# Kernel optimization log

Measured on AMD Instinct MI355X. Metric: run time of the kernel, lower is better.

## Reference

```python
import jax, jax.numpy as jnp
import numpy as np
import math

B, S, H, NH = 8, 1024, 1024, 16
DK = H // NH
EPS = 1e-6


def setup_inputs() -> dict:
    key = jax.random.key(0)
    ks = jax.random.split(key, 8)
    enc = jax.random.normal(ks[0], (B, S, H), dtype=jnp.float32)
    mask = jax.random.randint(ks[1], (B, 1, S, S), 0, 2, dtype=jnp.int32)
    scale = 1.0 / math.sqrt(H)
    W_Q = jax.random.normal(ks[2], (H, H), dtype=jnp.float32) * scale
    W_K = jax.random.normal(ks[3], (H, H), dtype=jnp.float32) * scale
    W_V = jax.random.normal(ks[4], (H, H), dtype=jnp.float32) * scale
    W_O = jax.random.normal(ks[5], (H, H), dtype=jnp.float32) * scale
    ln_gamma = jnp.ones((H,), dtype=jnp.float32)
    ln_beta = jnp.zeros((H,), dtype=jnp.float32)
    return {"enc": enc, "mask": mask, "W_Q": W_Q, "W_K": W_K, "W_V": W_V,
            "W_O": W_O, "ln_gamma": ln_gamma, "ln_beta": ln_beta}


def _layer_norm(x, gamma, beta):
    mu = jnp.mean(x, axis=-1, keepdims=True)
    var = jnp.mean(jnp.square(x - mu), axis=-1, keepdims=True)
    return (x - mu) / jnp.sqrt(var + EPS) * gamma + beta


def reference(enc, mask, W_Q, W_K, W_V, W_O, ln_gamma, ln_beta):
    # torch Linear: y = x @ W.T  (bias=False)
    # [B,S,H] -> [B,NH,S,DK]
    def heads(x, W):
        y = jnp.einsum('bsh,oh->bso', x, W)
        return y.reshape(B, S, NH, DK).transpose(0, 2, 1, 3)
    Q = heads(enc, W_Q)
    K = heads(enc, W_K)
    V = heads(enc, W_V)
    # attention scores [B,NH,S,S]
    scores = jnp.einsum('bhqd,bhkd->bhqk', Q, K) / math.sqrt(DK)
    scores = jnp.where(mask == 0, jnp.float32(-1e9), scores)
    attn_dist = jax.nn.softmax(scores, axis=-1)  # dropout_rate=0 -> no-op
    out = jnp.einsum('bhqk,bhkd->bhqd', attn_dist, V)
    out = out.transpose(0, 2, 1, 3).reshape(B, S, H)
    out = jnp.einsum('bsh,oh->bso', out, W_O)
    out = _layer_norm(out + enc, ln_gamma, ln_beta)
    return (out, attn_dist)
```

## Files before the change

kernel.cpp:

```cpp
#include <hip/hip_runtime.h>
#include <hip/hip_bf16.h>


typedef __bf16 bf16;
typedef __attribute__((ext_vector_type(8))) __bf16 bf16x8;
typedef __attribute__((ext_vector_type(4))) __bf16 bf16x4;
typedef __attribute__((ext_vector_type(4))) float f32x4;

#define MFMA16(a, b, c) __builtin_amdgcn_mfma_f32_16x16x32_bf16((a), (b), (c), 0, 0, 0)

#define B_ 8
#define S_ 1024
#define NH_ 16
#define DK_ 64
#define H_ 1024

#define SBAR()                                             \
  {                                                        \
    asm volatile("s_waitcnt lgkmcnt(0)" ::: "memory");     \
    __builtin_amdgcn_sched_barrier(0);                     \
    __builtin_amdgcn_s_barrier();                          \
    __builtin_amdgcn_sched_barrier(0);                     \
  }

__device__ __forceinline__ void gload_lds16b(const void* g, void* l) {
  __builtin_amdgcn_global_load_lds(
      (__attribute__((address_space(1))) void*)g,
      (__attribute__((address_space(3))) void*)l, 16, 0, 0);
}

__device__ __forceinline__ bf16x8 cat8(bf16x4 a, bf16x4 b) {
  bf16x8 r;
  r[0] = a[0]; r[1] = a[1]; r[2] = a[2]; r[3] = a[3];
  r[4] = b[0]; r[5] = b[1]; r[6] = b[2]; r[7] = b[3];
  return r;
}

__global__ __launch_bounds__(256) void cvt_all_kern(const float* __restrict__ enc,
                                                    const float* __restrict__ wq,
                                                    const float* __restrict__ wk,
                                                    const float* __restrict__ wv,
                                                    const float* __restrict__ wo_in,
                                                    const int* __restrict__ mask,
                                                    bf16* __restrict__ enc_bf,
                                                    bf16* __restrict__ wqkv,
                                                    bf16* __restrict__ wo,
                                                    unsigned char* __restrict__ mask8) {
  int i = blockIdx.x * 256 + threadIdx.x;
  if (i < 2097152) {
    float4 v = ((const float4*)enc)[i];
    bf16x4 o;
    o[0] = (bf16)v.x; o[1] = (bf16)v.y; o[2] = (bf16)v.z; o[3] = (bf16)v.w;
    ((bf16x4*)enc_bf)[i] = o;
  } else if (i < 3145728) {
    int j = i - 2097152;
    const float* src;
    bf16* dst;
    if (j < 262144) { src = wq; dst = (bf16*)wqkv; }
    else if (j < 524288) { src = wk; dst = wqkv + 1048576; j -= 262144; }
    else if (j < 786432) { src = wv; dst = wqkv + 2097152; j -= 524288; }
    else { src = wo_in; dst = wo; j -= 786432; }
    float4 v = ((const float4*)src)[j];
    bf16x4 o;
    o[0] = (bf16)v.x; o[1] = (bf16)v.y; o[2] = (bf16)v.z; o[3] = (bf16)v.w;
    ((bf16x4*)dst)[j] = o;
  } else {
    int j = i - 3145728;
    int4 v = ((const int4*)mask)[j];
    uchar4 o;
    o.x = (unsigned char)v.x; o.y = (unsigned char)v.y;
    o.z = (unsigned char)v.z; o.w = (unsigned char)v.w;
    ((uchar4*)mask8)[j] = o;
  }
}

__global__ __launch_bounds__(512, 2) void gemm256_kern(const bf16* __restrict__ A,
                                                       const bf16* __restrict__ Bt,
                                                       bf16* __restrict__ C,
                                                       int N, int NT) {
  __shared__ char Ab[2][32768];
  __shared__ char Bb[2][32768];
  const int nwg = gridDim.x;
  const int chunk = nwg >> 3;
  const int lin = blockIdx.x;
  const int v = (lin & 7) * chunk + (lin >> 3);
  const int tm = v / NT, tn = v % NT;
  const size_t m0 = (size_t)tm * 256, n0 = (size_t)tn * 256;
  const int t = threadIdx.x;
  const int l = t & 63, l15 = l & 15, lg = l >> 4;
  const int w = t >> 6, wr = w >> 2, wc = w & 3;

  const int row_t = t >> 3;
  const int scol = (((t & 7) ^ (row_t & 7)) << 4);
  const size_t Kb = 2048;
  const char* Ag = (const char*)A + (m0 + row_t) * Kb + scol;
  const char* Bg = (const char*)Bt + (n0 + row_t) * Kb + scol;
  const int dst = t * 16;

#define STAGE256(kt, buf)                                                        \
  {                                                                              \
    const size_t ko = (size_t)(kt) * 128;                                        \
    _Pragma("unroll") for (int ld = 0; ld < 4; ld++)                             \
        gload_lds16b(Ag + (size_t)ld * 64 * Kb + ko, &Ab[buf][ld * 8192 + dst]); \
    _Pragma("unroll") for (int ld = 0; ld < 4; ld++)                             \
        gload_lds16b(Bg + (size_t)ld * 64 * Kb + ko, &Bb[buf][ld * 8192 + dst]); \
  }

  const int sw = (l15 & 7) << 4;
  const int arowb = wr * 16384 + l15 * 128;
  const int browb = wc * 8192 + l15 * 128;

  f32x4 acc[8][4] = {};

  STAGE256(0, 0);
  STAGE256(1, 1);
  asm volatile("s_waitcnt vmcnt(8)" ::: "memory");
  __builtin_amdgcn_sched_barrier(0);
  __builtin_amdgcn_s_barrier();

  for (int it = 0; it < 16; ++it) {
    const int buf = it & 1;
#pragma unroll
    for (int kk = 0; kk < 2; kk++) {
      bf16x8 a[8], b[4];
#pragma unroll
      for (int i = 0; i < 8; i++)
        a[i] = *(const bf16x8*)&Ab[buf][arowb + i * 2048 + ((kk * 64 + lg * 16) ^ sw)];
#pragma unroll
      for (int n = 0; n < 4; n++)
        b[n] = *(const bf16x8*)&Bb[buf][browb + n * 2048 + ((kk * 64 + lg * 16) ^ sw)];
      __builtin_amdgcn_s_setprio(1);
#pragma unroll
      for (int i = 0; i < 8; i++)
#pragma unroll
        for (int n = 0; n < 4; n++) acc[i][n] = MFMA16(a[i], b[n], acc[i][n]);
      __builtin_amdgcn_s_setprio(0);
    }
    asm volatile("s_waitcnt lgkmcnt(0)" ::: "memory");
    __builtin_amdgcn_sched_barrier(0);
    __builtin_amdgcn_s_barrier();
    if (it < 14) STAGE256(it + 2, buf);
    if (it < 15) {
      if (it == 14) {
        asm volatile("s_waitcnt vmcnt(0)" ::: "memory");
      } else {
        asm volatile("s_waitcnt vmcnt(8)" ::: "memory");
      }
      __builtin_amdgcn_sched_barrier(0);
      __builtin_amdgcn_s_barrier();
    }
  }

#pragma unroll
  for (int i = 0; i < 8; i++)
#pragma unroll
    for (int n = 0; n < 4; n++)
#pragma unroll
      for (int j = 0; j < 4; j++) {
        size_t row = m0 + wr * 128 + i * 16 + lg * 4 + j;
        size_t col = n0 + wc * 64 + n * 16 + l15;
        C[row * (size_t)N + col] = (bf16)acc[i][n][j];
      }
#undef STAGE256
}

template <bool F32OUT>
__global__ __launch_bounds__(256) void gemm_bt_kern(const bf16* __restrict__ A,
                                                    const bf16* __restrict__ Bt,
                                                    void* __restrict__ Cout,
                                                    const float* __restrict__ resid,
                                                    int K, int ldc) {
  __shared__ bf16 As[128 * 32];
  __shared__ bf16 Bs[128 * 32];
  const int lin = blockIdx.y * gridDim.x + blockIdx.x;
  const int nwg = gridDim.x * gridDim.y;
  const int chunk = nwg >> 3;
  const int v = (lin & 7) * chunk + (lin >> 3);
  const int m0 = (v / gridDim.x) * 128, n0 = (v % gridDim.x) * 128;
  const int tid = threadIdx.x;
  const int w = tid >> 6, l = tid & 63, l15 = l & 15, lg = l >> 4;
  const int wm = w >> 1, wn = w & 1;

  const bf16* Ab = A + (size_t)(m0 + (tid >> 2)) * K + (tid & 3) * 8;
  const bf16* Bb = Bt + (size_t)(n0 + (tid >> 2)) * K + (tid & 3) * 8;
  char* AsB = (char*)As + tid * 16;
  char* BsB = (char*)Bs + tid * 16;

  f32x4 acc[4][4] = {};
  for (int k0 = 0; k0 < K; k0 += 32) {
    gload_lds16b(Ab + k0, AsB);
    gload_lds16b(Ab + (size_t)64 * K + k0, AsB + 4096);
    gload_lds16b(Bb + k0, BsB);
    gload_lds16b(Bb + (size_t)64 * K + k0, BsB + 4096);
    __syncthreads();
    bf16x8 af[4], bfv[4];
#pragma unroll
    for (int m = 0; m < 4; m++)
      af[m] = *(const bf16x8*)&As[(wm * 64 + m * 16 + l15) * 32 + lg * 8];
#pragma unroll
    for (int n = 0; n < 4; n++)
      bfv[n] = *(const bf16x8*)&Bs[(wn * 64 + n * 16 + l15) * 32 + lg * 8];
#pragma unroll
    for (int m = 0; m < 4; m++)
#pragma unroll
      for (int n = 0; n < 4; n++) acc[m][n] = MFMA16(af[m], bfv[n], acc[m][n]);
    __syncthreads();
  }
#pragma unroll
  for (int m = 0; m < 4; m++)
#pragma unroll
    for (int n = 0; n < 4; n++)
#pragma unroll
      for (int j = 0; j < 4; j++) {
        int row = m0 + wm * 64 + m * 16 + lg * 4 + j;
        int col = n0 + wn * 64 + n * 16 + l15;
        if constexpr (F32OUT) {
          ((float*)Cout)[(size_t)row * ldc + col] =
              acc[m][n][j] + resid[(size_t)row * ldc + col];
        } else {
          ((bf16*)Cout)[(size_t)row * ldc + col] = (bf16)acc[m][n][j];
        }
      }
}

__global__ __launch_bounds__(256) void vtrans_kern(const bf16* __restrict__ qkv,
                                                   bf16* __restrict__ vT) {
  int blk = blockIdx.x;
  int st = blk & 15;
  int h = (blk >> 4) & 15;
  int b = blk >> 8;
  __shared__ bf16 t[64][65];
  int tid = threadIdx.x;
  {
    int r = tid >> 2, cb = (tid & 3) * 16;
    const bf16* src = qkv + ((size_t)(b * S_ + st * 64 + r)) * 3072 + 2048 + h * DK_ + cb;
    bf16x8 u0 = *(const bf16x8*)src;
    bf16x8 u1 = *(const bf16x8*)(src + 8);
#pragma unroll
    for (int j = 0; j < 8; j++) { t[r][cb + j] = u0[j]; t[r][cb + 8 + j] = u1[j]; }
  }
  __syncthreads();
  {
    int d = tid >> 2, sb = (tid & 3) * 16;
    bf16* dst = vT + ((size_t)((b * NH_ + h) * DK_ + d)) * S_ + st * 64 + sb;
#pragma unroll
    for (int j = 0; j < 16; j++) dst[j] = t[sb + j][d];
  }
}

#define PSTR 2056
#define MSTR 1032
#define KSTR 136

__global__ __launch_bounds__(512, 2) void attn_fused(const bf16* __restrict__ qkv,
                                                     const bf16* __restrict__ vT,
                                                     const unsigned char* __restrict__ mask8,
                                                     float* __restrict__ attn_out,
                                                     bf16* __restrict__ ctx) {
  __shared__ char smem[78848];
  char* Pb = smem;
  char* stg = smem + 65792;
  char* qtl = smem + 74496;
  float* red = (float*)(smem + 74496);

  const int vb = (blockIdx.x & 7) * 512 + (blockIdx.x >> 3);
  const int qt = vb & 31, h = (vb >> 5) & 15, b = vb >> 9;
  const int q0 = qt * 32;
  const int t = threadIdx.x;
  const int w = t >> 6, l = t & 63, l15 = l & 15, lg = l >> 4;
  const int qsub = w >> 2, ksub = w & 3;
  const int qrow = qsub * 16 + l15;

  const char* qkv_b = (const char*)qkv;
  const char* kb_g = qkv_b + (size_t)b * S_ * 6144 + 2048 + (size_t)h * 128;
  const char* vT_b = (const char*)vT + (size_t)(b * NH_ + h) * 64 * 2048;
  const unsigned char* mrow = mask8 + (size_t)b * S_ * S_ + (size_t)q0 * S_;

  const int srow = t >> 3, scol = (t & 7) * 16;

  uint4 qreg, mreg[4], kr0, kr1;
  if (t < 256) {
    int row = t >> 3;
    qreg = *(const uint4*)(qkv_b + (size_t)(b * S_ + q0 + row) * 6144 + h * 128 + scol);
  }
#pragma unroll
  for (int p = 0; p < 4; p++) {
    int row = (t >> 6) + p * 8, col = (t & 63) * 16;
    mreg[p] = *(const uint4*)(mrow + (size_t)row * 1024 + col);
  }
  kr0 = *(const uint4*)(kb_g + (size_t)srow * 6144 + scol);
  kr1 = *(const uint4*)(kb_g + (size_t)(64 + srow) * 6144 + scol);

  if (t < 256) {
    int row = t >> 3;
    *(uint2*)(qtl + row * KSTR + scol) = make_uint2(qreg.x, qreg.y);
    *(uint2*)(qtl + row * KSTR + scol + 8) = make_uint2(qreg.z, qreg.w);
  }
#pragma unroll
  for (int p = 0; p < 4; p++) {
    int row = (t >> 6) + p * 8, col = (t & 63) * 16;
    *(uint2*)(Pb + row * MSTR + col) = make_uint2(mreg[p].x, mreg[p].y);
    *(uint2*)(Pb + row * MSTR + col + 8) = make_uint2(mreg[p].z, mreg[p].w);
  }
  *(uint2*)(stg + srow * KSTR + scol) = make_uint2(kr0.x, kr0.y);
  *(uint2*)(stg + srow * KSTR + scol + 8) = make_uint2(kr0.z, kr0.w);
  __syncthreads();

  bf16x8 aq[2];
#pragma unroll
  for (int kk = 0; kk < 2; kk++) {
    bf16x4 a0 = *(bf16x4*)(qtl + qrow * KSTR + kk * 64 + lg * 16);
    bf16x4 a1 = *(bf16x4*)(qtl + qrow * KSTR + kk * 64 + lg * 16 + 8);
    aq[kk] = cat8(a0, a1);
  }

  f32x4 sc[16];
#pragma unroll
  for (int i = 0; i < 16; i++) sc[i] = (f32x4){0.f, 0.f, 0.f, 0.f};
  uint4 kr[2];
  kr[1] = kr1;
  const int krow = ksub * 16 + l15;
#pragma unroll
  for (int cc = 0; cc < 16; cc++) {
    if (cc < 14)
      kr[cc & 1] = *(const uint4*)(kb_g + (size_t)((cc + 2) * 64 + srow) * 6144 + scol);
#pragma unroll
    for (int kk = 0; kk < 2; kk++) {
      bf16x4 b0 = *(bf16x4*)(stg + krow * KSTR + kk * 64 + lg * 16);
      bf16x4 b1 = *(bf16x4*)(stg + krow * KSTR + kk * 64 + lg * 16 + 8);
      sc[cc] = MFMA16(cat8(b0, b1), aq[kk], sc[cc]);
    }
    SBAR();
    if (cc < 15) {
      uint4 kw = kr[(cc + 1) & 1];
      *(uint2*)(stg + srow * KSTR + scol) = make_uint2(kw.x, kw.y);
      *(uint2*)(stg + srow * KSTR + scol + 8) = make_uint2(kw.z, kw.w);
      SBAR();
    }
  }

  const float SCL = 0.125f * 1.44269504f;
  float rmax = -3e38f;
#pragma unroll
  for (int cc = 0; cc < 16; cc++) {
    int kb4 = cc * 64 + ksub * 16 + lg * 4;
    uchar4 mv = *(const uchar4*)(Pb + qrow * MSTR + kb4);
    unsigned char mb[4] = {mv.x, mv.y, mv.z, mv.w};
#pragma unroll
    for (int j = 0; j < 4; j++) {
      float s = sc[cc][j] * SCL;
      if (mb[j] == 0) s = -1e9f;
      sc[cc][j] = s;
      rmax = fmaxf(rmax, s);
    }
  }
  rmax = fmaxf(rmax, __shfl_xor(rmax, 16));
  rmax = fmaxf(rmax, __shfl_xor(rmax, 32));
  float rsum = 0.f;
#pragma unroll
  for (int cc = 0; cc < 16; cc++)
#pragma unroll
    for (int j = 0; j < 4; j++) {
      float e = exp2f(sc[cc][j] - rmax);
      sc[cc][j] = e;
      rsum += e;
    }
  rsum += __shfl_xor(rsum, 16);
  rsum += __shfl_xor(rsum, 32);
  if (lg == 0) {
    red[(w * 32 + qrow) * 2] = rmax;
    red[(w * 32 + qrow) * 2 + 1] = rsum;
  }
  SBAR();
  float gm = -3e38f, gs = 0.f;
  const int g4 = qsub * 4;
#pragma unroll
  for (int i = 0; i < 4; i++) gm = fmaxf(gm, red[((g4 + i) * 32 + qrow) * 2]);
#pragma unroll
  for (int i = 0; i < 4; i++)
    gs += red[((g4 + i) * 32 + qrow) * 2 + 1] * exp2f(red[((g4 + i) * 32 + qrow) * 2] - gm);
  const float scale = exp2f(rmax - gm) / gs;

#pragma unroll
  for (int cc = 0; cc < 16; cc++) {
    bf16x4 pb;
#pragma unroll
    for (int j = 0; j < 4; j++) pb[j] = (bf16)(sc[cc][j] * scale);
    *(bf16x4*)(Pb + qrow * PSTR + cc * 128 + ksub * 32 + lg * 8) = pb;
  }
  uint4 vr[2];
  vr[0] = *(const uint4*)(vT_b + (size_t)srow * 2048 + scol);
  vr[1] = *(const uint4*)(vT_b + (size_t)srow * 2048 + 128 + scol);
  SBAR();
  *(uint2*)(stg + srow * KSTR + scol) = make_uint2(vr[0].x, vr[0].y);
  *(uint2*)(stg + srow * KSTR + scol + 8) = make_uint2(vr[0].z, vr[0].w);
  SBAR();

  f32x4 o = {0.f, 0.f, 0.f, 0.f};
  const int dkr = ksub * 16 + l15;
#pragma unroll
  for (int cc = 0; cc < 16; cc++) {
    if (cc < 14)
      vr[cc & 1] = *(const uint4*)(vT_b + (size_t)srow * 2048 + (cc + 2) * 128 + scol);
#pragma unroll
    for (int tt = 0; tt < 2; tt++) {
      bf16x4 p0 = *(bf16x4*)(Pb + qrow * PSTR + cc * 128 + tt * 64 + lg * 16);
      bf16x4 p1 = *(bf16x4*)(Pb + qrow * PSTR + cc * 128 + tt * 64 + lg * 16 + 8);
      bf16x4 v0 = *(bf16x4*)(stg + dkr * KSTR + tt * 64 + lg * 16);
      bf16x4 v1 = *(bf16x4*)(stg + dkr * KSTR + tt * 64 + lg * 16 + 8);
      o = MFMA16(cat8(p0, p1), cat8(v0, v1), o);
    }
    SBAR();
    if (cc < 15) {
      uint4 vw = vr[(cc + 1) & 1];
      *(uint2*)(stg + srow * KSTR + scol) = make_uint2(vw.x, vw.y);
      *(uint2*)(stg + srow * KSTR + scol + 8) = make_uint2(vw.z, vw.w);
      SBAR();
    }
  }

  {
    int row = t >> 4, c16 = t & 15;
    float* arow = attn_out + (size_t)((b * NH_ + h) * S_ + q0 + row) * S_;
#pragma unroll
    for (int it = 0; it < 16; it++) {
      bf16x4 pv = *(bf16x4*)(Pb + row * PSTR + c16 * 8 + it * 128);
      f32x4 o4;
#pragma unroll
      for (int j = 0; j < 4; j++) o4[j] = (float)pv[j];
      __builtin_nontemporal_store(o4, (f32x4*)(arow + c16 * 4 + it * 64));
    }
  }

#pragma unroll
  for (int jj = 0; jj < 4; jj++) {
    int row = qsub * 16 + lg * 4 + jj;
    *(bf16*)(stg + row * KSTR + (ksub * 16 + l15) * 2) = (bf16)o[jj];
  }
  SBAR();
  if (t < 256) {
    int row = t >> 3;
    bf16x4 c0 = *(bf16x4*)(stg + row * KSTR + scol);
    bf16x4 c1 = *(bf16x4*)(stg + row * KSTR + scol + 8);
    bf16x8 cv = cat8(c0, c1);
    *(bf16x8*)((char*)ctx + (size_t)(b * S_ + q0 + row) * 2048 + h * 128 + scol) = cv;
  }
}

__global__ __launch_bounds__(256) void ln_kern(float* __restrict__ y,
                                               const float* __restrict__ gamma,
                                               const float* __restrict__ beta) {
  int row = blockIdx.x;
  int tid = threadIdx.x;
  float4 v = *(const float4*)&y[(size_t)row * 1024 + tid * 4];
  float s = v.x + v.y + v.z + v.w;
  float q = v.x * v.x + v.y * v.y + v.z * v.z + v.w * v.w;
#pragma unroll
  for (int m = 1; m < 64; m <<= 1) { s += __shfl_xor(s, m); q += __shfl_xor(q, m); }
  __shared__ float rb[8];
  if ((tid & 63) == 0) { rb[(tid >> 6) * 2] = s; rb[(tid >> 6) * 2 + 1] = q; }
  __syncthreads();
  s = rb[0] + rb[2] + rb[4] + rb[6];
  q = rb[1] + rb[3] + rb[5] + rb[7];
  float mu = s * (1.f / 1024.f);
  float var = q * (1.f / 1024.f) - mu * mu;
  float rstd = rsqrtf(var + 1e-6f);
  float4 g = *(const float4*)&gamma[tid * 4];
  float4 bb = *(const float4*)&beta[tid * 4];
  float4 o;
  o.x = (v.x - mu) * rstd * g.x + bb.x;
  o.y = (v.y - mu) * rstd * g.y + bb.y;
  o.z = (v.z - mu) * rstd * g.z + bb.z;
  o.w = (v.w - mu) * rstd * g.w + bb.w;
  *(float4*)&y[(size_t)row * 1024 + tid * 4] = o;
}

extern "C" void kernel_launch(void* const* d_in, const int* in_sizes, int n_in,
                              void* d_out, int out_size, void* d_ws, size_t ws_size,
                              hipStream_t stream) {
  const float* enc = (const float*)d_in[0];
  const int* mask = (const int*)d_in[1];
  const float* W_Q = (const float*)d_in[2];
  const float* W_K = (const float*)d_in[3];
  const float* W_V = (const float*)d_in[4];
  const float* W_O = (const float*)d_in[5];
  const float* ln_g = (const float*)d_in[6];
  const float* ln_b = (const float*)d_in[7];

  float* out_f32 = (float*)d_out;
  float* attn_f32 = (float*)d_out + (size_t)B_ * S_ * H_;

  char* wsb = (char*)d_ws;
  bf16* enc_bf = (bf16*)wsb;
  bf16* wqkv = (bf16*)(wsb + 16777216);
  bf16* wo = (bf16*)(wsb + 23068672);
  bf16* qkv = (bf16*)(wsb + 25165824);
  bf16* vT = (bf16*)(wsb + 75497472);
  bf16* ctx = (bf16*)(wsb + 92274688);
  unsigned char* mask8 = (unsigned char*)(wsb + 109051904);

  cvt_all_kern<<<20480, 256, 0, stream>>>(enc, W_Q, W_K, W_V, W_O, mask,
                                          enc_bf, wqkv, wo, mask8);

  gemm256_kern<<<384, 512, 0, stream>>>(enc_bf, wqkv, qkv, 3072, 12);

  vtrans_kern<<<2048, 256, 0, stream>>>(qkv, vT);

  attn_fused<<<4096, 512, 0, stream>>>(qkv, vT, mask8, attn_f32, ctx);

  gemm_bt_kern<true><<<dim3(8, 64), 256, 0, stream>>>(ctx, wo, out_f32, enc, 1024, 1024);

  ln_kern<<<8192, 256, 0, stream>>>(out_f32, ln_g, ln_b);
}
```

Before: 305.6 us.

## Restructure attention kernel around per-wave private K/V staging with swizzled LDS

Each wave now computes scores for its own 128-key slice across all 32 query rows. It streams K and V tiles through a private, XOR-swizzled 2 KB LDS slice. This removes the block-wide barriers that the shared staging buffer needed on every iteration of the QK and PV loops. The probability tile in LDS is also XOR-swizzled instead of padded, to avoid bank conflicts. The launch bound now requests 4 blocks per CU, which tightens the register budget while each thread holds 64 score accumulators, so spills are a risk; the larger LDS footprint may also cap occupancy.

```diff
diff --git a/kernel.cpp b/kernel.cpp
--- a/kernel.cpp
+++ b/kernel.cpp
@@ -15,12 +15,12 @@
 #define DK_ 64
 #define H_ 1024
 
-#define SBAR()                                             \
-  {                                                        \
-    asm volatile("s_waitcnt lgkmcnt(0)" ::: "memory");     \
-    __builtin_amdgcn_sched_barrier(0);                     \
-    __builtin_amdgcn_s_barrier();                          \
-    __builtin_amdgcn_sched_barrier(0);                     \
+#define SBAR()                                         \
+  {                                                    \
+    asm volatile("s_waitcnt lgkmcnt(0)" ::: "memory"); \
+    __builtin_amdgcn_sched_barrier(0);                 \
+    __builtin_amdgcn_s_barrier();                      \
+    __builtin_amdgcn_sched_barrier(0);                 \
   }
 
 __device__ __forceinline__ void gload_lds16b(const void* g, void* l) {
@@ -248,183 +248,217 @@
   }
 }
 
-#define PSTR 2056
-#define MSTR 1032
-#define KSTR 136
-
-__global__ __launch_bounds__(512, 2) void attn_fused(const bf16* __restrict__ qkv,
-                                                     const bf16* __restrict__ vT,
-                                                     const unsigned char* __restrict__ mask8,
-                                                     float* __restrict__ attn_out,
-                                                     bf16* __restrict__ ctx) {
-  __shared__ char smem[78848];
+__global__ __launch_bounds__(512, 4) void attn_wp(const bf16* __restrict__ qkv,
+                                                  const bf16* __restrict__ vT,
+                                                  const unsigned char* __restrict__ mask8,
+                                                  float* __restrict__ attn_out,
+                                                  bf16* __restrict__ ctx) {
+  __shared__ char smem[81920];
   char* Pb = smem;
-  char* stg = smem + 65792;
-  char* qtl = smem + 74496;
-  float* red = (float*)(smem + 74496);
+  char* mk = smem;
+  char* qtl = smem + 36864;
+  float* red = (float*)(smem + 45056);
+  char* stg = smem + 65536;
 
   const int vb = (blockIdx.x & 7) * 512 + (blockIdx.x >> 3);
   const int qt = vb & 31, h = (vb >> 5) & 15, b = vb >> 9;
   const int q0 = qt * 32;
   const int t = threadIdx.x;
   const int w = t >> 6, l = t & 63, l15 = l & 15, lg = l >> 4;
-  const int qsub = w >> 2, ksub = w & 3;
-  const int qrow = qsub * 16 + l15;
+  const int qsub = w >> 2, dkq = w & 3;
 
   const char* qkv_b = (const char*)qkv;
   const char* kb_g = qkv_b + (size_t)b * S_ * 6144 + 2048 + (size_t)h * 128;
   const char* vT_b = (const char*)vT + (size_t)(b * NH_ + h) * 64 * 2048;
   const unsigned char* mrow = mask8 + (size_t)b * S_ * S_ + (size_t)q0 * S_;
 
-  const int srow = t >> 3, scol = (t & 7) * 16;
-
-  uint4 qreg, mreg[4], kr0, kr1;
+  char* myst = stg + w * 2048;
+  const int sr = l >> 3;
+  const int sc8 = (l & 7) * 2;
+
+#define WSLICE(vv, row)                                              \
+  {                                                                  \
+    *(uint2*)(myst + (row) * 128 + 8 * (sc8 ^ (row))) =              \
+        make_uint2((vv).x, (vv).y);                                  \
+    *(uint2*)(myst + (row) * 128 + 8 * ((sc8 + 1) ^ (row))) =        \
+        make_uint2((vv).z, (vv).w);                                  \
+  }
+
+  uint4 qreg, mreg[4];
   if (t < 256) {
-    int row = t >> 3;
-    qreg = *(const uint4*)(qkv_b + (size_t)(b * S_ + q0 + row) * 6144 + h * 128 + scol);
+    int row = t >> 3, c = (t & 7) * 16;
+    qreg = *(const uint4*)(qkv_b + (size_t)(b * S_ + q0 + row) * 6144 + h * 128 + c);
   }
 #pragma unroll
   for (int p = 0; p < 4; p++) {
     int row = (t >> 6) + p * 8, col = (t & 63) * 16;
     mreg[p] = *(const uint4*)(mrow + (size_t)row * 1024 + col);
   }
-  kr0 = *(const uint4*)(kb_g + (size_t)srow * 6144 + scol);
-  kr1 = *(const uint4*)(kb_g + (size_t)(64 + srow) * 6144 + scol);
+  uint4 ka = *(const uint4*)(kb_g + (size_t)(w * 128 + sr) * 6144 + (l & 7) * 16);
+  uint4 kb2 = *(const uint4*)(kb_g + (size_t)(w * 128 + 8 + sr) * 6144 + (l & 7) * 16);
 
   if (t < 256) {
-    int row = t >> 3;
-    *(uint2*)(qtl + row * KSTR + scol) = make_uint2(qreg.x, qreg.y);
-    *(uint2*)(qtl + row * KSTR + scol + 8) = make_uint2(qreg.z, qreg.w);
+    int row = t >> 3, c = (t & 7) * 16;
+    *(uint2*)(qtl + row * 136 + c) = make_uint2(qreg.x, qreg.y);
+    *(uint2*)(qtl + row * 136 + c + 8) = make_uint2(qreg.z, qreg.w);
   }
 #pragma unroll
   for (int p = 0; p < 4; p++) {
     int row = (t >> 6) + p * 8, col = (t & 63) * 16;
-    *(uint2*)(Pb + row * MSTR + col) = make_uint2(mreg[p].x, mreg[p].y);
-    *(uint2*)(Pb + row * MSTR + col + 8) = make_uint2(mreg[p].z, mreg[p].w);
-  }
-  *(uint2*)(stg + srow * KSTR + scol) = make_uint2(kr0.x, kr0.y);
-  *(uint2*)(stg + srow * KSTR + scol + 8) = make_uint2(kr0.z, kr0.w);
-  __syncthreads();
-
-  bf16x8 aq[2];
-#pragma unroll
-  for (int kk = 0; kk < 2; kk++) {
-    bf16x4 a0 = *(bf16x4*)(qtl + qrow * KSTR + kk * 64 + lg * 16);
-    bf16x4 a1 = *(bf16x4*)(qtl + qrow * KSTR + kk * 64 + lg * 16 + 8);
-    aq[kk] = cat8(a0, a1);
-  }
-
-  f32x4 sc[16];
-#pragma unroll
-  for (int i = 0; i < 16; i++) sc[i] = (f32x4){0.f, 0.f, 0.f, 0.f};
-  uint4 kr[2];
-  kr[1] = kr1;
-  const int krow = ksub * 16 + l15;
-#pragma unroll
-  for (int cc = 0; cc < 16; cc++) {
-    if (cc < 14)
-      kr[cc & 1] = *(const uint4*)(kb_g + (size_t)((cc + 2) * 64 + srow) * 6144 + scol);
+    *(uint2*)(mk + row * 1032 + col) = make_uint2(mreg[p].x, mreg[p].y);
+    *(uint2*)(mk + row * 1032 + col + 8) = make_uint2(mreg[p].z, mreg[p].w);
+  }
+  WSLICE(ka, sr);
+  WSLICE(kb2, sr + 8);
+  SBAR();
+
+  bf16x8 aq[2][2];
+#pragma unroll
+  for (int qm = 0; qm < 2; qm++)
 #pragma unroll
     for (int kk = 0; kk < 2; kk++) {
-      bf16x4 b0 = *(bf16x4*)(stg + krow * KSTR + kk * 64 + lg * 16);
-      bf16x4 b1 = *(bf16x4*)(stg + krow * KSTR + kk * 64 + lg * 16 + 8);
-      sc[cc] = MFMA16(cat8(b0, b1), aq[kk], sc[cc]);
-    }
-    SBAR();
+      int row = qm * 16 + l15;
+      bf16x4 a0 = *(bf16x4*)(qtl + row * 136 + kk * 64 + lg * 16);
+      bf16x4 a1 = *(bf16x4*)(qtl + row * 136 + kk * 64 + lg * 16 + 8);
+      aq[qm][kk] = cat8(a0, a1);
+    }
+
+  f32x4 sc[8][2] = {};
+  uint4 nka, nkb;
+#pragma unroll
+  for (int sub = 0; sub < 8; ++sub) {
+    if (sub < 7) {
+      nka = *(const uint4*)(kb_g + (size_t)(w * 128 + (sub + 1) * 16 + sr) * 6144 + (l & 7) * 16);
+      nkb = *(const uint4*)(kb_g + (size_t)(w * 128 + (sub + 1) * 16 + 8 + sr) * 6144 + (l & 7) * 16);
+    }
+#pragma unroll
+    for (int kk = 0; kk < 2; kk++) {
+      int c8a = kk * 8 + lg * 2;
+      bf16x4 f0 = *(bf16x4*)(myst + l15 * 128 + 8 * (c8a ^ l15));
+      bf16x4 f1 = *(bf16x4*)(myst + l15 * 128 + 8 * ((c8a + 1) ^ l15));
+      bf16x8 kf = cat8(f0, f1);
+      sc[sub][0] = MFMA16(kf, aq[0][kk], sc[sub][0]);
+      sc[sub][1] = MFMA16(kf, aq[1][kk], sc[sub][1]);
+    }
+    if (sub < 7) {
+      WSLICE(nka, sr);
+      WSLICE(nkb, sr + 8);
+    }
+  }
+
+  const float SCL = 0.125f * 1.44269504f;
+  float rmax[2] = {-3e38f, -3e38f};
+#pragma unroll
+  for (int sub = 0; sub < 8; ++sub)
+#pragma unroll
+    for (int qm = 0; qm < 2; qm++) {
+      int qrow2 = qm * 16 + l15;
+      uchar4 mv = *(const uchar4*)(mk + qrow2 * 1032 + w * 128 + sub * 16 + lg * 4);
+      unsigned char mb[4] = {mv.x, mv.y, mv.z, mv.w};
+#pragma unroll
+      for (int j = 0; j < 4; j++) {
+        float s = sc[sub][qm][j] * SCL;
+        if (mb[j] == 0) s = -1e9f;
+        sc[sub][qm][j] = s;
+        rmax[qm] = fmaxf(rmax[qm], s);
+      }
+    }
+#pragma unroll
+  for (int qm = 0; qm < 2; qm++) {
+    float v = rmax[qm];
+    v = fmaxf(v, __shfl_xor(v, 16));
+    v = fmaxf(v, __shfl_xor(v, 32));
+    rmax[qm] = v;
+  }
+  float rsum[2] = {0.f, 0.f};
+#pragma unroll
+  for (int sub = 0; sub < 8; ++sub)
+#pragma unroll
+    for (int qm = 0; qm < 2; qm++)
+#pragma unroll
+      for (int j = 0; j < 4; j++) {
+        float e = exp2f(sc[sub][qm][j] - rmax[qm]);
+        sc[sub][qm][j] = e;
+        rsum[qm] += e;
+      }
+#pragma unroll
+  for (int qm = 0; qm < 2; qm++) {
+    float v = rsum[qm];
+    v += __shfl_xor(v, 16);
+    v += __shfl_xor(v, 32);
+    rsum[qm] = v;
+  }
+  if (lg == 0) {
+#pragma unroll
+    for (int qm = 0; qm < 2; qm++) {
+      red[(w * 32 + qm * 16 + l15) * 2] = rmax[qm];
+      red[(w * 32 + qm * 16 + l15) * 2 + 1] = rsum[qm];
+    }
+  }
+  SBAR();
+  float scale[2];
+#pragma unroll
+  for (int qm = 0; qm < 2; qm++) {
+    int qrow2 = qm * 16 + l15;
+    float gm = -3e38f, gs = 0.f;
+#pragma unroll
+    for (int i = 0; i < 8; i++) gm = fmaxf(gm, red[(i * 32 + qrow2) * 2]);
+#pragma unroll
+    for (int i = 0; i < 8; i++)
+      gs += red[(i * 32 + qrow2) * 2 + 1] * exp2f(red[(i * 32 + qrow2) * 2] - gm);
+    scale[qm] = exp2f(rmax[qm] - gm) / gs;
+  }
+  SBAR();
+
+  uint4 va = *(const uint4*)(vT_b + (size_t)(dkq * 16 + sr) * 2048 + (l & 7) * 16);
+  uint4 vb2 = *(const uint4*)(vT_b + (size_t)(dkq * 16 + 8 + sr) * 2048 + (l & 7) * 16);
+#pragma unroll
+  for (int sub = 0; sub < 8; ++sub)
+#pragma unroll
+    for (int qm = 0; qm < 2; qm++) {
+      int row = qm * 16 + l15;
+      bf16x4 pb;
+#pragma unroll
+      for (int j = 0; j < 4; j++) pb[j] = (bf16)(sc[sub][qm][j] * scale[qm]);
+      *(bf16x4*)(Pb + (size_t)row * 2048 +
+                 ((w * 256 + sub * 32 + lg * 8) ^ ((row & 7) << 4))) = pb;
+    }
+  WSLICE(va, sr);
+  WSLICE(vb2, sr + 8);
+  SBAR();
+
+  f32x4 o = {0.f, 0.f, 0.f, 0.f};
+  const size_t prb = (size_t)(qsub * 16 + l15) * 2048;
+  const int psw = ((qsub * 16 + l15) & 7) << 4;
+  uint4 nva, nvb;
+#pragma unroll
+  for (int cc = 0; cc < 16; ++cc) {
     if (cc < 15) {
-      uint4 kw = kr[(cc + 1) & 1];
-      *(uint2*)(stg + srow * KSTR + scol) = make_uint2(kw.x, kw.y);
-      *(uint2*)(stg + srow * KSTR + scol + 8) = make_uint2(kw.z, kw.w);
-      SBAR();
-    }
-  }
-
-  const float SCL = 0.125f * 1.44269504f;
-  float rmax = -3e38f;
-#pragma unroll
-  for (int cc = 0; cc < 16; cc++) {
-    int kb4 = cc * 64 + ksub * 16 + lg * 4;
-    uchar4 mv = *(const uchar4*)(Pb + qrow * MSTR + kb4);
-    unsigned char mb[4] = {mv.x, mv.y, mv.z, mv.w};
-#pragma unroll
-    for (int j = 0; j < 4; j++) {
-      float s = sc[cc][j] * SCL;
-      if (mb[j] == 0) s = -1e9f;
-      sc[cc][j] = s;
-      rmax = fmaxf(rmax, s);
-    }
-  }
-  rmax = fmaxf(rmax, __shfl_xor(rmax, 16));
-  rmax = fmaxf(rmax, __shfl_xor(rmax, 32));
-  float rsum = 0.f;
-#pragma unroll
-  for (int cc = 0; cc < 16; cc++)
-#pragma unroll
-    for (int j = 0; j < 4; j++) {
-      float e = exp2f(sc[cc][j] - rmax);
-      sc[cc][j] = e;
-      rsum += e;
-    }
-  rsum += __shfl_xor(rsum, 16);
-  rsum += __shfl_xor(rsum, 32);
-  if (lg == 0) {
-    red[(w * 32 + qrow) * 2] = rmax;
-    red[(w * 32 + qrow) * 2 + 1] = rsum;
+      nva = *(const uint4*)(vT_b + (size_t)(dkq * 16 + sr) * 2048 + (cc + 1) * 128 + (l & 7) * 16);
+      nvb = *(const uint4*)(vT_b + (size_t)(dkq * 16 + 8 + sr) * 2048 + (cc + 1) * 128 + (l & 7) * 16);
+    }
+#pragma unroll
+    for (int tt = 0; tt < 2; tt++) {
+      bf16x8 pf = *(const bf16x8*)(Pb + prb + ((cc * 128 + tt * 64 + lg * 16) ^ psw));
+      int c8a = tt * 8 + lg * 2;
+      bf16x4 v0 = *(bf16x4*)(myst + l15 * 128 + 8 * (c8a ^ l15));
+      bf16x4 v1 = *(bf16x4*)(myst + l15 * 128 + 8 * ((c8a + 1) ^ l15));
+      o = MFMA16(pf, cat8(v0, v1), o);
+    }
+    if (cc < 15) {
+      WSLICE(nva, sr);
+      WSLICE(nvb, sr + 8);
+    }
   }
   SBAR();
-  float gm = -3e38f, gs = 0.f;
-  const int g4 = qsub * 4;
-#pragma unroll
-  for (int i = 0; i < 4; i++) gm = fmaxf(gm, red[((g4 + i) * 32 + qrow) * 2]);
-#pragma unroll
-  for (int i = 0; i < 4; i++)
-    gs += red[((g4 + i) * 32 + qrow) * 2 + 1] * exp2f(red[((g4 + i) * 32 + qrow) * 2] - gm);
-  const float scale = exp2f(rmax - gm) / gs;
-
-#pragma unroll
-  for (int cc = 0; cc < 16; cc++) {
-    bf16x4 pb;
-#pragma unroll
-    for (int j = 0; j < 4; j++) pb[j] = (bf16)(sc[cc][j] * scale);
-    *(bf16x4*)(Pb + qrow * PSTR + cc * 128 + ksub * 32 + lg * 8) = pb;
-  }
-  uint4 vr[2];
-  vr[0] = *(const uint4*)(vT_b + (size_t)srow * 2048 + scol);
-  vr[1] = *(const uint4*)(vT_b + (size_t)srow * 2048 + 128 + scol);
-  SBAR();
-  *(uint2*)(stg + srow * KSTR + scol) = make_uint2(vr[0].x, vr[0].y);
-  *(uint2*)(stg + srow * KSTR + scol + 8) = make_uint2(vr[0].z, vr[0].w);
-  SBAR();
-
-  f32x4 o = {0.f, 0.f, 0.f, 0.f};
-  const int dkr = ksub * 16 + l15;
-#pragma unroll
-  for (int cc = 0; cc < 16; cc++) {
-    if (cc < 14)
-      vr[cc & 1] = *(const uint4*)(vT_b + (size_t)srow * 2048 + (cc + 2) * 128 + scol);
-#pragma unroll
-    for (int tt = 0; tt < 2; tt++) {
-      bf16x4 p0 = *(bf16x4*)(Pb + qrow * PSTR + cc * 128 + tt * 64 + lg * 16);
-      bf16x4 p1 = *(bf16x4*)(Pb + qrow * PSTR + cc * 128 + tt * 64 + lg * 16 + 8);
-      bf16x4 v0 = *(bf16x4*)(stg + dkr * KSTR + tt * 64 + lg * 16);
-      bf16x4 v1 = *(bf16x4*)(stg + dkr * KSTR + tt * 64 + lg * 16 + 8);
-      o = MFMA16(cat8(p0, p1), cat8(v0, v1), o);
-    }
-    SBAR();
-    if (cc < 15) {
-      uint4 vw = vr[(cc + 1) & 1];
-      *(uint2*)(stg + srow * KSTR + scol) = make_uint2(vw.x, vw.y);
-      *(uint2*)(stg + srow * KSTR + scol + 8) = make_uint2(vw.z, vw.w);
-      SBAR();
-    }
-  }
 
   {
     int row = t >> 4, c16 = t & 15;
+    int rsw = (row & 7) << 4;
     float* arow = attn_out + (size_t)((b * NH_ + h) * S_ + q0 + row) * S_;
 #pragma unroll
     for (int it = 0; it < 16; it++) {
-      bf16x4 pv = *(bf16x4*)(Pb + row * PSTR + c16 * 8 + it * 128);
+      bf16x4 pv = *(bf16x4*)(Pb + (size_t)row * 2048 + ((c16 * 8 + it * 128) ^ rsw));
       f32x4 o4;
 #pragma unroll
       for (int j = 0; j < 4; j++) o4[j] = (float)pv[j];
@@ -435,16 +469,17 @@
 #pragma unroll
   for (int jj = 0; jj < 4; jj++) {
     int row = qsub * 16 + lg * 4 + jj;
-    *(bf16*)(stg + row * KSTR + (ksub * 16 + l15) * 2) = (bf16)o[jj];
+    *(bf16*)(stg + row * 136 + (dkq * 16 + l15) * 2) = (bf16)o[jj];
   }
   SBAR();
   if (t < 256) {
-    int row = t >> 3;
-    bf16x4 c0 = *(bf16x4*)(stg + row * KSTR + scol);
-    bf16x4 c1 = *(bf16x4*)(stg + row * KSTR + scol + 8);
+    int row = t >> 3, c = (t & 7) * 16;
+    bf16x4 c0 = *(bf16x4*)(stg + row * 136 + c);
+    bf16x4 c1 = *(bf16x4*)(stg + row * 136 + c + 8);
     bf16x8 cv = cat8(c0, c1);
-    *(bf16x8*)((char*)ctx + (size_t)(b * S_ + q0 + row) * 2048 + h * 128 + scol) = cv;
-  }
+    *(bf16x8*)((char*)ctx + (size_t)(b * S_ + q0 + row) * 2048 + h * 128 + c) = cv;
+  }
+#undef WSLICE
 }
 
 __global__ __launch_bounds__(256) void ln_kern(float* __restrict__ y,
@@ -506,7 +541,7 @@
 
   vtrans_kern<<<2048, 256, 0, stream>>>(qkv, vT);
 
-  attn_fused<<<4096, 512, 0, stream>>>(qkv, vT, mask8, attn_f32, ctx);
+  attn_wp<<<4096, 512, 0, stream>>>(qkv, vT, mask8, attn_f32, ctx);
 
   gemm_bt_kern<true><<<dim3(8, 64), 256, 0, stream>>>(ctx, wo, out_f32, enc, 1024, 1024);
 
```

New measurement: 359.1 us. 1.17x slower.
